# Kernel optimization log

Hardware: AMD Instinct MI355X
Metric: run time of the kernel (lower is better)

The kernel has to match this reference:

```python
import jax, jax.numpy as jnp
import numpy as np

DIM = 256
HID = 1024
BATCH = 16384
STEP_SIZE = 0.1
NSTEPS = 10  # int(1.0 / step_size)


def setup_inputs() -> dict:
    key = jax.random.key(0)
    ks = jax.random.split(key, 8)
    x = jax.random.normal(ks[0], (BATCH, DIM), dtype=jnp.float32)
    # Scaled init so tanh layers stay in a sane range (like default torch init).
    W1 = jax.random.normal(ks[1], (DIM + 1, HID), dtype=jnp.float32) / np.sqrt(DIM + 1)
    b1 = jnp.zeros((HID,), dtype=jnp.float32)
    W2 = jax.random.normal(ks[2], (HID, HID), dtype=jnp.float32) / np.sqrt(HID)
    b2 = jnp.zeros((HID,), dtype=jnp.float32)
    W3 = jax.random.normal(ks[3], (HID, DIM), dtype=jnp.float32) / np.sqrt(HID)
    b3 = jnp.zeros((DIM,), dtype=jnp.float32)
    proj_mat = jax.random.normal(ks[4], (DIM, DIM), dtype=jnp.float32)
    return {"x": x, "W1": W1, "b1": b1, "W2": W2, "b2": b2,
            "W3": W3, "b3": b3, "proj_mat": proj_mat}


def reference(x, W1, b1, W2, b2, W3, b3, proj_mat):
    """FlowProposal.log_prob: backward RK4 integration of dx/dt = v(x,t)
    from t=1 to t=0 with Hutchinson trace estimation via forward-mode JVP.
    Returns log q(x), shape [batch]."""
    dtype = x.dtype

    def net(xc, t):
        # VelocityMLP: concat(x, t) -> tanh MLP -> velocity [B, DIM]
        tcol = jnp.broadcast_to(jnp.asarray(t, dtype), (xc.shape[0], 1))
        h = jnp.tanh(jnp.concatenate([xc, tcol], axis=1) @ W1 + b1)
        h = jnp.tanh(h @ W2 + b2)
        return h @ W3 + b3

    # Deterministic hashed Hutchinson noise (from the INITIAL x, as in torch).
    noise = jnp.sin((x @ proj_mat) * 1000.0) * 1.41421356  # sqrt(2)

    def dyn(xc, t):
        v, jv = jax.jvp(lambda xi: net(xi, t), (xc,), (noise,))
        tr = jnp.sum(noise * jv, axis=1, keepdims=True)  # eps^T J eps, [B,1]
        return v, tr

    dt = -STEP_SIZE

    def step(carry, k):
        xt, ljt = carry
        t = 1.0 + dt * k
        v1, tr1 = dyn(xt, t)
        v2, tr2 = dyn(xt + dt * 0.5 * v1, t + dt * 0.5)
        v3, tr3 = dyn(xt + dt * 0.5 * v2, t + dt * 0.5)
        v4, tr4 = dyn(xt + dt * v3, t + dt)
        xt = xt + (dt / 6.0) * (v1 + 2 * v2 + 2 * v3 + v4)
        ljt = ljt + (dt / 6.0) * (tr1 + 2 * tr2 + 2 * tr3 + tr4)
        return (xt, ljt), None

    init = (x, jnp.zeros((x.shape[0], 1), dtype))
    (xt, ljt), _ = jax.lax.scan(step, init, jnp.arange(NSTEPS, dtype=dtype))

    log_prob_z = -0.5 * jnp.sum(xt * xt, axis=1) - 0.5 * DIM * jnp.log(jnp.asarray(2.0 * np.pi, dtype))
    return log_prob_z - ljt[:, 0]
```

## Files before the change

kernel.cpp:

```cpp
#include <hip/hip_runtime.h>
#include <stdint.h>
#include <stddef.h>

typedef unsigned short ushort_t;
typedef float f32x4 __attribute__((ext_vector_type(4)));
typedef short short8 __attribute__((ext_vector_type(8)));

#define NB 16384
#define DIMX 256
#define HIDX 1024
#define DTC (-0.1f)

__device__ __forceinline__ unsigned short f2bf_bits(float f){
  unsigned int u = __float_as_uint(f);
  unsigned int r = (u + 0x7FFFu + ((u >> 16) & 1u)) >> 16;
  return (unsigned short)r;
}
__device__ __forceinline__ float bf2f_bits(unsigned short s){
  return __uint_as_float(((unsigned int)s) << 16);
}
__device__ __forceinline__ float fast_tanh(float x){
  float a = fabsf(x);
  float e = __expf(a + a);
  float r = 1.0f - 2.0f / (e + 1.0f);
  return copysignf(r, x);
}
__device__ __forceinline__ void gload16(const void* g, void* l){
  __builtin_amdgcn_global_load_lds(
      (const __attribute__((address_space(1))) void*)g,
      (__attribute__((address_space(3))) void*)l, 16, 0, 0);
}
template<int N> __device__ __forceinline__ void wait_vmcnt(){
  if constexpr (N == 0)      asm volatile("s_waitcnt vmcnt(0)" ::: "memory");
  else if constexpr (N == 4) asm volatile("s_waitcnt vmcnt(4)" ::: "memory");
  else if constexpr (N == 6) asm volatile("s_waitcnt vmcnt(6)" ::: "memory");
  else if constexpr (N == 8) asm volatile("s_waitcnt vmcnt(8)" ::: "memory");
  else static_assert(N == 0, "unsupported vmcnt");
}
__device__ __forceinline__ int ldsx(int r, int c){
  return r * 64 + (c ^ ((r & 7) << 3));
}

__global__ void prep_weights(const float* __restrict__ W1, const float* __restrict__ W2,
                             const float* __restrict__ W3,
                             ushort_t* __restrict__ W1at, ushort_t* __restrict__ W2t,
                             ushort_t* __restrict__ W3t, ushort_t* __restrict__ W3n){
  int i = blockIdx.x * blockDim.x + threadIdx.x;
  const int T1 = 1024 * 256, T2 = 1024 * 1024, T3 = 256 * 1024, T4 = 1024 * 256;
  if (i < T1){
    int n = i >> 8, k = i & 255;
    W1at[i] = f2bf_bits(W1[k * 1024 + n]);
  } else if (i < T1 + T2){
    int j = i - T1; int n = j >> 10, k = j & 1023;
    W2t[j] = f2bf_bits(W2[k * 1024 + n]);
  } else if (i < T1 + T2 + T3){
    int j = i - T1 - T2; int n = j >> 10, k = j & 1023;
    W3t[j] = f2bf_bits(W3[k * 256 + n]);
  } else if (i < T1 + T2 + T3 + T4){
    int j = i - T1 - T2 - T3;
    W3n[j] = f2bf_bits(W3[j]);
  }
}

__global__ void noise_init(const float* __restrict__ x, const float* __restrict__ proj,
                           ushort_t* __restrict__ noise_bf,
                           float* __restrict__ xt, ushort_t* __restrict__ xcbf,
                           float* __restrict__ ljt){
  const int r0 = blockIdx.x * 8;
  const int j = threadIdx.x;
  __shared__ float xrow[8][256];
  #pragma unroll
  for (int r = 0; r < 8; ++r) xrow[r][j] = x[(size_t)(r0 + r) * 256 + j];
  __syncthreads();
  float s[8] = {0.f,0.f,0.f,0.f,0.f,0.f,0.f,0.f};
  for (int k = 0; k < 256; ++k){
    float p = proj[k * 256 + j];
    #pragma unroll
    for (int r = 0; r < 8; ++r) s[r] = fmaf(xrow[r][k], p, s[r]);
  }
  #pragma unroll
  for (int r = 0; r < 8; ++r){
    float nz = sinf(s[r] * 1000.0f) * 1.41421356237f;
    size_t idx = (size_t)(r0 + r) * 256 + j;
    noise_bf[idx] = f2bf_bits(nz);
    float xv = xrow[r][j];
    xt[idx] = xv;
    xcbf[idx] = f2bf_bits(xv);
  }
  if (j < 8) ljt[r0 + j] = 0.0f;
}

template<int BM, int BN, int WGM, int K, int DUAL, int EPI, int PIPE>
__launch_bounds__(512, 2)
__global__ void gemm_kernel(const ushort_t* __restrict__ A1, const ushort_t* __restrict__ A2,
                            const ushort_t* __restrict__ Wt,
                            ushort_t* __restrict__ out1, ushort_t* __restrict__ out2,
                            const float* __restrict__ bias, const float* __restrict__ w1trow,
                            float tval,
                            const ushort_t* __restrict__ dz1,
                            const ushort_t* __restrict__ gtr,
                            float* __restrict__ xt, float* __restrict__ vacc,
                            ushort_t* __restrict__ xcbf,
                            float* __restrict__ ljt, float wdt6, int rk){
  constexpr int BK = 64;
  constexpr int WGN = 8 / WGM;
  constexpr int WM = BM / WGM, WN = BN / WGN;
  constexpr int M_REP = WM / 16, N_REP = WN / 16;
  constexpr int ATILES = DUAL ? 2 : 1;
  constexpr int CH_A = BM / 8;
  constexpr int CH_TOT = ATILES * CH_A + BN / 8;
  constexpr int CH_PW = CH_TOT / 8;
  constexpr int BUF_E = (ATILES * BM + BN) * BK;
  constexpr int NBUF = PIPE ? 2 : 1;
  constexpr int NK = K / BK;
  static_assert(!PIPE || NK >= 2, "pipeline needs >=2 K-steps");

  __shared__ __align__(16) ushort_t lds[NBUF * BUF_E];

  const int m0 = blockIdx.x * BM;
  const int n0 = blockIdx.y * BN;
  const int tid = threadIdx.x;
  const int lane = tid & 63;
  const int wid = tid >> 6;
  const int wr = wid / WGN;
  const int wc = wid % WGN;

  f32x4 acc1[M_REP][N_REP] = {};
  f32x4 acc2[M_REP][N_REP] = {};

  const int srow = lane >> 3;
  const int scol = ((lane & 7) ^ srow) * 8;

  const ushort_t* srcb[CH_PW];
  #pragma unroll
  for (int c = 0; c < CH_PW; ++c){
    const int ch = wid * CH_PW + c;
    if (ch < CH_A)
      srcb[c] = A1 + (size_t)(m0 + ch * 8 + srow) * K + scol;
    else if (DUAL && ch < 2 * CH_A)
      srcb[c] = A2 + (size_t)(m0 + (ch - CH_A) * 8 + srow) * K + scol;
    else
      srcb[c] = Wt + (size_t)(n0 + (ch - ATILES * CH_A) * 8 + srow) * K + scol;
  }

  auto do_stage = [&](int buf, int ks){
    ushort_t* dst = lds + buf * BUF_E + (wid * CH_PW) * 512;
    const int k0 = ks * BK;
    #pragma unroll
    for (int c = 0; c < CH_PW; ++c)
      gload16(srcb[c] + k0, dst + c * 512);
  };

  auto compute = [&](int buf){
    const ushort_t* ldsA1 = lds + buf * BUF_E;
    const ushort_t* ldsA2 = ldsA1 + BM * BK;
    const ushort_t* ldsB  = ldsA1 + ATILES * BM * BK;
    #pragma unroll
    for (int kk = 0; kk < 2; ++kk){
      short8 a1f[M_REP], a2f[M_REP], bfr[N_REP];
      const int lco = kk * 32 + (lane >> 4) * 8;
      const int lro = lane & 15;
      #pragma unroll
      for (int m = 0; m < M_REP; ++m){
        int r = wr * WM + m * 16 + lro;
        a1f[m] = *(const short8*)(ldsA1 + ldsx(r, lco));
        if (DUAL) a2f[m] = *(const short8*)(ldsA2 + ldsx(r, lco));
      }
      #pragma unroll
      for (int n = 0; n < N_REP; ++n){
        int cN = wc * WN + n * 16 + lro;
        bfr[n] = *(const short8*)(ldsB + ldsx(cN, lco));
      }
      #pragma unroll
      for (int m = 0; m < M_REP; ++m){
        #pragma unroll
        for (int n = 0; n < N_REP; ++n){
          acc1[m][n] = __builtin_amdgcn_mfma_f32_16x16x32_bf16(a1f[m], bfr[n], acc1[m][n], 0, 0, 0);
          if (DUAL)
            acc2[m][n] = __builtin_amdgcn_mfma_f32_16x16x32_bf16(a2f[m], bfr[n], acc2[m][n], 0, 0, 0);
        }
      }
    }
  };

  if constexpr (PIPE){
    do_stage(0, 0);
    do_stage(1, 1);
    for (int ks = 0; ks < NK - 2; ++ks){
      wait_vmcnt<CH_PW>();
      __builtin_amdgcn_s_barrier();
      compute(ks & 1);
      asm volatile("s_waitcnt lgkmcnt(0)" ::: "memory");
      __builtin_amdgcn_s_barrier();
      do_stage(ks & 1, ks + 2);
    }
    wait_vmcnt<CH_PW>();
    __builtin_amdgcn_s_barrier();
    compute(NK & 1);
    wait_vmcnt<0>();
    __builtin_amdgcn_s_barrier();
    compute((NK - 1) & 1);
  } else {
    for (int ks = 0; ks < NK; ++ks){
      do_stage(0, ks);
      __syncthreads();
      compute(0);
      __syncthreads();
    }
  }

  const int rbase = (lane >> 4) * 4;
  const int cbase = lane & 15;
  if (EPI <= 1){
    #pragma unroll
    for (int m = 0; m < M_REP; ++m){
      #pragma unroll
      for (int n = 0; n < N_REP; ++n){
        #pragma unroll
        for (int j = 0; j < 4; ++j){
          const int R = m0 + wr * WM + m * 16 + rbase + j;
          const int C = n0 + wc * WN + n * 16 + cbase;
          const size_t idx = (size_t)R * HIDX + C;
          float a = acc1[m][n][j];
          if (EPI == 0){
            out1[idx] = f2bf_bits(a);
          } else {
            float z = a + bias[C] + tval * w1trow[C];
            float h = fast_tanh(z);
            out1[idx] = f2bf_bits(h);
            float d = bf2f_bits(dz1[idx]);
            out2[idx] = f2bf_bits(fmaf(-h, h, 1.0f) * d);
          }
        }
      }
    }
  } else if (EPI == 2){
    #pragma unroll
    for (int m = 0; m < M_REP; ++m){
      #pragma unroll
      for (int j = 0; j < 4; ++j){
        const int R = m0 + wr * WM + m * 16 + rbase + j;
        float psum = 0.0f;
        #pragma unroll
        for (int n = 0; n < N_REP; ++n){
          const int C = n0 + wc * WN + n * 16 + cbase;
          const size_t idx = (size_t)R * HIDX + C;
          float h = fast_tanh(acc1[m][n][j] + bias[C]);
          out1[idx] = f2bf_bits(h);
          float dh2 = fmaf(-h, h, 1.0f) * acc2[m][n][j];
          psum += dh2 * bf2f_bits(gtr[idx]);
        }
        #pragma unroll
        for (int off = 1; off < 16; off <<= 1) psum += __shfl_xor(psum, off, 64);
        if (cbase == 0) atomicAdd(&ljt[R], wdt6 * psum);
      }
    }
  } else {
    #pragma unroll
    for (int m = 0; m < M_REP; ++m){
      #pragma unroll
      for (int n = 0; n < N_REP; ++n){
        #pragma unroll
        for (int j = 0; j < 4; ++j){
          const int R = m0 + wr * WM + m * 16 + rbase + j;
          const int C = n0 + wc * WN + n * 16 + cbase;
          const size_t idx = (size_t)R * DIMX + C;
          float v = acc1[m][n][j] + bias[C];
          float xtv = xt[idx];
          if (rk == 0){
            vacc[idx] = v;
            xcbf[idx] = f2bf_bits(xtv + 0.5f * DTC * v);
          } else if (rk == 1){
            vacc[idx] += 2.0f * v;
            xcbf[idx] = f2bf_bits(xtv + 0.5f * DTC * v);
          } else if (rk == 2){
            vacc[idx] += 2.0f * v;
            xcbf[idx] = f2bf_bits(xtv + DTC * v);
          } else {
            float xtn = xtv + (DTC / 6.0f) * (vacc[idx] + v);
            xt[idx] = xtn;
            xcbf[idx] = f2bf_bits(xtn);
          }
        }
      }
    }
  }
}

__global__ void final_kernel(const float* __restrict__ xt, const float* __restrict__ ljt,
                             float* __restrict__ out){
  const int row = blockIdx.x * 4 + (threadIdx.x >> 6);
  const int lane = threadIdx.x & 63;
  const float4 xv = *(const float4*)(xt + (size_t)row * 256 + lane * 4);
  float s = xv.x * xv.x + xv.y * xv.y + xv.z * xv.z + xv.w * xv.w;
  #pragma unroll
  for (int off = 32; off; off >>= 1) s += __shfl_xor(s, off, 64);
  if (lane == 0) out[row] = -0.5f * s - 235.2482645f - ljt[row];
}

extern "C" void kernel_launch(void* const* d_in, const int* in_sizes, int n_in,
                              void* d_out, int out_size, void* d_ws, size_t ws_size,
                              hipStream_t stream){
  (void)in_sizes; (void)n_in; (void)out_size; (void)ws_size;
  const float* x    = (const float*)d_in[0];
  const float* W1   = (const float*)d_in[1];
  const float* b1   = (const float*)d_in[2];
  const float* W2   = (const float*)d_in[3];
  const float* b2   = (const float*)d_in[4];
  const float* W3   = (const float*)d_in[5];
  const float* b3   = (const float*)d_in[6];
  const float* proj = (const float*)d_in[7];

  size_t off = 0;
  char* wsb = (char*)d_ws;
  auto carve = [&](size_t n) -> char* {
    char* p = wsb + off; off += (n + 255) & ~(size_t)255; return p;
  };
  ushort_t* W1at     = (ushort_t*)carve((size_t)1024 * 256 * 2);
  ushort_t* W2t      = (ushort_t*)carve((size_t)1024 * 1024 * 2);
  ushort_t* W3t      = (ushort_t*)carve((size_t)256 * 1024 * 2);
  ushort_t* W3n      = (ushort_t*)carve((size_t)1024 * 256 * 2);
  ushort_t* noise_bf = (ushort_t*)carve((size_t)NB * 256 * 2);
  ushort_t* dz1      = (ushort_t*)carve((size_t)NB * 1024 * 2);
  ushort_t* gtr      = (ushort_t*)carve((size_t)NB * 1024 * 2);
  float*    xt       = (float*)carve((size_t)NB * 256 * 4);
  ushort_t* xcbf     = (ushort_t*)carve((size_t)NB * 256 * 2);
  float*    vacc     = (float*)carve((size_t)NB * 256 * 4);
  float*    ljt      = (float*)carve((size_t)NB * 4);
  ushort_t* h1       = (ushort_t*)carve((size_t)NB * 1024 * 2);
  ushort_t* dh1      = (ushort_t*)carve((size_t)NB * 1024 * 2);
  ushort_t* h2       = (ushort_t*)carve((size_t)NB * 1024 * 2);

  prep_weights<<<7168, 256, 0, stream>>>(W1, W2, W3, W1at, W2t, W3t, W3n);
  noise_init<<<NB / 8, 256, 0, stream>>>(x, proj, noise_bf, xt, xcbf, ljt);

  gemm_kernel<256, 256, 2, 256, 0, 0, 0><<<dim3(NB / 256, 4), 512, 0, stream>>>(
      noise_bf, nullptr, W1at, dz1, nullptr, nullptr, nullptr, 0.f,
      nullptr, nullptr, nullptr, nullptr, nullptr, nullptr, 0.f, 0);
  gemm_kernel<256, 256, 2, 256, 0, 0, 0><<<dim3(NB / 256, 4), 512, 0, stream>>>(
      noise_bf, nullptr, W3n, gtr, nullptr, nullptr, nullptr, 0.f,
      nullptr, nullptr, nullptr, nullptr, nullptr, nullptr, 0.f, 0);

  const float toff[4] = {0.0f, -0.05f, -0.05f, -0.1f};
  const float wst[4]  = {1.0f, 2.0f, 2.0f, 1.0f};
  for (int k = 0; k < 10; ++k){
    float t = 1.0f - 0.1f * (float)k;
    for (int s = 0; s < 4; ++s){
      gemm_kernel<256, 256, 2, 256, 0, 1, 0><<<dim3(NB / 256, 4), 512, 0, stream>>>(
          xcbf, nullptr, W1at, h1, dh1, b1, W1 + 256 * 1024, t + toff[s],
          dz1, nullptr, nullptr, nullptr, nullptr, nullptr, 0.f, 0);
      gemm_kernel<128, 256, 2, 1024, 1, 2, 1><<<dim3(NB / 128, 4), 512, 0, stream>>>(
          h1, dh1, W2t, h2, nullptr, b2, nullptr, 0.f,
          nullptr, gtr, nullptr, nullptr, nullptr, ljt, wst[s] * (DTC / 6.0f), 0);
      gemm_kernel<128, 128, 4, 1024, 0, 3, 0><<<dim3(NB / 128, 2), 512, 0, stream>>>(
          h2, nullptr, W3t, nullptr, nullptr, b3, nullptr, 0.f,
          nullptr, nullptr, xt, vacc, xcbf, nullptr, 0.f, s);
    }
  }
  final_kernel<<<NB / 4, 256, 0, stream>>>(xt, ljt, (float*)d_out);
}
```

Baseline: 5.661 ms.

## Add BK=32 pipelined path for dual-A W2 GEMM with smaller tiles, higher occupancy

Adds a new pipeline mode for the dual-input (h1, dh1) W2 GEMM that stages 32-wide K slices into a double-buffered LDS tile with a new XOR swizzle. The launch switches from 128x256 tiles to 128x128 tiles and doubles the grid, with launch bounds raised to allow four blocks per CU. The goal is to cut per-block LDS and registers so more blocks can be resident and hide latency. The cost is that each A tile is loaded twice as often across the N dimension, and there are more barriers per unit of K work.

```diff
diff --git a/kernel.cpp b/kernel.cpp
--- a/kernel.cpp
+++ b/kernel.cpp
@@ -32,6 +32,7 @@
 }
 template<int N> __device__ __forceinline__ void wait_vmcnt(){
   if constexpr (N == 0)      asm volatile("s_waitcnt vmcnt(0)" ::: "memory");
+  else if constexpr (N == 3) asm volatile("s_waitcnt vmcnt(3)" ::: "memory");
   else if constexpr (N == 4) asm volatile("s_waitcnt vmcnt(4)" ::: "memory");
   else if constexpr (N == 6) asm volatile("s_waitcnt vmcnt(6)" ::: "memory");
   else if constexpr (N == 8) asm volatile("s_waitcnt vmcnt(8)" ::: "memory");
@@ -39,6 +40,9 @@
 }
 __device__ __forceinline__ int ldsx(int r, int c){
   return r * 64 + (c ^ ((r & 7) << 3));
+}
+__device__ __forceinline__ int ldsx32(int r, int g){
+  return r * 32 + ((g ^ (r & 3) ^ ((r >> 2) & 3)) << 3);
 }
 
 __global__ void prep_weights(const float* __restrict__ W1, const float* __restrict__ W2,
@@ -91,7 +95,7 @@
 }
 
 template<int BM, int BN, int WGM, int K, int DUAL, int EPI, int PIPE>
-__launch_bounds__(512, 2)
+__launch_bounds__(512, (PIPE == 3) ? 4 : 2)
 __global__ void gemm_kernel(const ushort_t* __restrict__ A1, const ushort_t* __restrict__ A2,
                             const ushort_t* __restrict__ Wt,
                             ushort_t* __restrict__ out1, ushort_t* __restrict__ out2,
@@ -102,20 +106,11 @@
                             float* __restrict__ xt, float* __restrict__ vacc,
                             ushort_t* __restrict__ xcbf,
                             float* __restrict__ ljt, float wdt6, int rk){
-  constexpr int BK = 64;
   constexpr int WGN = 8 / WGM;
   constexpr int WM = BM / WGM, WN = BN / WGN;
   constexpr int M_REP = WM / 16, N_REP = WN / 16;
   constexpr int ATILES = DUAL ? 2 : 1;
-  constexpr int CH_A = BM / 8;
-  constexpr int CH_TOT = ATILES * CH_A + BN / 8;
-  constexpr int CH_PW = CH_TOT / 8;
-  constexpr int BUF_E = (ATILES * BM + BN) * BK;
-  constexpr int NBUF = PIPE ? 2 : 1;
-  constexpr int NK = K / BK;
-  static_assert(!PIPE || NK >= 2, "pipeline needs >=2 K-steps");
-
-  __shared__ __align__(16) ushort_t lds[NBUF * BUF_E];
+  constexpr int ROWS = ATILES * BM + BN;
 
   const int m0 = blockIdx.x * BM;
   const int n0 = blockIdx.y * BN;
@@ -128,84 +123,158 @@
   f32x4 acc1[M_REP][N_REP] = {};
   f32x4 acc2[M_REP][N_REP] = {};
 
-  const int srow = lane >> 3;
-  const int scol = ((lane & 7) ^ srow) * 8;
-
-  const ushort_t* srcb[CH_PW];
-  #pragma unroll
-  for (int c = 0; c < CH_PW; ++c){
-    const int ch = wid * CH_PW + c;
-    if (ch < CH_A)
-      srcb[c] = A1 + (size_t)(m0 + ch * 8 + srow) * K + scol;
-    else if (DUAL && ch < 2 * CH_A)
-      srcb[c] = A2 + (size_t)(m0 + (ch - CH_A) * 8 + srow) * K + scol;
-    else
-      srcb[c] = Wt + (size_t)(n0 + (ch - ATILES * CH_A) * 8 + srow) * K + scol;
-  }
-
-  auto do_stage = [&](int buf, int ks){
-    ushort_t* dst = lds + buf * BUF_E + (wid * CH_PW) * 512;
-    const int k0 = ks * BK;
-    #pragma unroll
-    for (int c = 0; c < CH_PW; ++c)
-      gload16(srcb[c] + k0, dst + c * 512);
-  };
-
-  auto compute = [&](int buf){
-    const ushort_t* ldsA1 = lds + buf * BUF_E;
-    const ushort_t* ldsA2 = ldsA1 + BM * BK;
-    const ushort_t* ldsB  = ldsA1 + ATILES * BM * BK;
-    #pragma unroll
-    for (int kk = 0; kk < 2; ++kk){
+  if constexpr (PIPE == 3){
+    constexpr int NT = K / 32;
+    constexpr int CH = ROWS / 16;
+    constexpr int CH_PW = CH / 8;
+    constexpr int BUF_E = ROWS * 32;
+    static_assert(CH_PW * 8 == CH, "chunk split");
+    __shared__ __align__(16) ushort_t lds[2 * BUF_E];
+
+    const int srow = lane >> 2;
+    const int scb  = (lane & 3) ^ (srow & 3) ^ ((srow >> 2) & 3);
+    const int scol = scb << 3;
+    const ushort_t* srcb[CH_PW];
+    #pragma unroll
+    for (int c = 0; c < CH_PW; ++c){
+      const int gr = (wid * CH_PW + c) * 16 + srow;
+      if (gr < BM)               srcb[c] = A1 + (size_t)(m0 + gr) * K + scol;
+      else if (DUAL && gr < 2 * BM) srcb[c] = A2 + (size_t)(m0 + gr - BM) * K + scol;
+      else                       srcb[c] = Wt + (size_t)(n0 + gr - ATILES * BM) * K + scol;
+    }
+    auto do_stage = [&](int buf, int t){
+      ushort_t* dst = lds + buf * BUF_E + (wid * CH_PW) * 512;
+      #pragma unroll
+      for (int c = 0; c < CH_PW; ++c)
+        gload16(srcb[c] + t * 32, dst + c * 512);
+    };
+    auto compute = [&](int buf){
+      const ushort_t* base = lds + buf * BUF_E;
+      const int g = lane >> 4;
+      const int lro = lane & 15;
       short8 a1f[M_REP], a2f[M_REP], bfr[N_REP];
-      const int lco = kk * 32 + (lane >> 4) * 8;
-      const int lro = lane & 15;
       #pragma unroll
       for (int m = 0; m < M_REP; ++m){
-        int r = wr * WM + m * 16 + lro;
-        a1f[m] = *(const short8*)(ldsA1 + ldsx(r, lco));
-        if (DUAL) a2f[m] = *(const short8*)(ldsA2 + ldsx(r, lco));
+        const int r = wr * WM + m * 16 + lro;
+        a1f[m] = *(const short8*)(base + ldsx32(r, g));
+        a2f[m] = *(const short8*)(base + ldsx32(BM + r, g));
       }
       #pragma unroll
       for (int n = 0; n < N_REP; ++n){
-        int cN = wc * WN + n * 16 + lro;
-        bfr[n] = *(const short8*)(ldsB + ldsx(cN, lco));
+        const int rn = ATILES * BM + wc * WN + n * 16 + lro;
+        bfr[n] = *(const short8*)(base + ldsx32(rn, g));
       }
       #pragma unroll
       for (int m = 0; m < M_REP; ++m){
         #pragma unroll
         for (int n = 0; n < N_REP; ++n){
           acc1[m][n] = __builtin_amdgcn_mfma_f32_16x16x32_bf16(a1f[m], bfr[n], acc1[m][n], 0, 0, 0);
-          if (DUAL)
-            acc2[m][n] = __builtin_amdgcn_mfma_f32_16x16x32_bf16(a2f[m], bfr[n], acc2[m][n], 0, 0, 0);
-        }
-      }
-    }
-  };
-
-  if constexpr (PIPE){
+          acc2[m][n] = __builtin_amdgcn_mfma_f32_16x16x32_bf16(a2f[m], bfr[n], acc2[m][n], 0, 0, 0);
+        }
+      }
+    };
     do_stage(0, 0);
     do_stage(1, 1);
-    for (int ks = 0; ks < NK - 2; ++ks){
+    for (int t = 0; t < NT - 2; ++t){
       wait_vmcnt<CH_PW>();
       __builtin_amdgcn_s_barrier();
-      compute(ks & 1);
+      compute(t & 1);
       asm volatile("s_waitcnt lgkmcnt(0)" ::: "memory");
       __builtin_amdgcn_s_barrier();
-      do_stage(ks & 1, ks + 2);
+      do_stage(t & 1, t + 2);
     }
     wait_vmcnt<CH_PW>();
     __builtin_amdgcn_s_barrier();
-    compute(NK & 1);
+    compute(NT & 1);
     wait_vmcnt<0>();
     __builtin_amdgcn_s_barrier();
-    compute((NK - 1) & 1);
+    compute((NT - 1) & 1);
   } else {
-    for (int ks = 0; ks < NK; ++ks){
-      do_stage(0, ks);
-      __syncthreads();
-      compute(0);
-      __syncthreads();
+    constexpr int BK = 64;
+    constexpr int CH_A = BM / 8;
+    constexpr int CH_TOT = ATILES * CH_A + BN / 8;
+    constexpr int CH_PW = CH_TOT / 8;
+    constexpr int BUF_E = ROWS * BK;
+    constexpr int NBUF = PIPE ? 2 : 1;
+    constexpr int NK = K / BK;
+    __shared__ __align__(16) ushort_t lds[NBUF * BUF_E];
+
+    const int srow = lane >> 3;
+    const int scol = ((lane & 7) ^ srow) * 8;
+    const ushort_t* srcb[CH_PW];
+    #pragma unroll
+    for (int c = 0; c < CH_PW; ++c){
+      const int ch = wid * CH_PW + c;
+      if (ch < CH_A)
+        srcb[c] = A1 + (size_t)(m0 + ch * 8 + srow) * K + scol;
+      else if (DUAL && ch < 2 * CH_A)
+        srcb[c] = A2 + (size_t)(m0 + (ch - CH_A) * 8 + srow) * K + scol;
+      else
+        srcb[c] = Wt + (size_t)(n0 + (ch - ATILES * CH_A) * 8 + srow) * K + scol;
+    }
+    auto do_stage = [&](int buf, int ks){
+      ushort_t* dst = lds + buf * BUF_E + (wid * CH_PW) * 512;
+      const int k0 = ks * BK;
+      #pragma unroll
+      for (int c = 0; c < CH_PW; ++c)
+        gload16(srcb[c] + k0, dst + c * 512);
+    };
+    auto compute = [&](int buf){
+      const ushort_t* ldsA1 = lds + buf * BUF_E;
+      const ushort_t* ldsA2 = ldsA1 + BM * BK;
+      const ushort_t* ldsB  = ldsA1 + ATILES * BM * BK;
+      #pragma unroll
+      for (int kk = 0; kk < 2; ++kk){
+        short8 a1f[M_REP], a2f[M_REP], bfr[N_REP];
+        const int lco = kk * 32 + (lane >> 4) * 8;
+        const int lro = lane & 15;
+        #pragma unroll
+        for (int m = 0; m < M_REP; ++m){
+          int r = wr * WM + m * 16 + lro;
+          a1f[m] = *(const short8*)(ldsA1 + ldsx(r, lco));
+          if (DUAL) a2f[m] = *(const short8*)(ldsA2 + ldsx(r, lco));
+        }
+        #pragma unroll
+        for (int n = 0; n < N_REP; ++n){
+          int cN = wc * WN + n * 16 + lro;
+          bfr[n] = *(const short8*)(ldsB + ldsx(cN, lco));
+        }
+        #pragma unroll
+        for (int m = 0; m < M_REP; ++m){
+          #pragma unroll
+          for (int n = 0; n < N_REP; ++n){
+            acc1[m][n] = __builtin_amdgcn_mfma_f32_16x16x32_bf16(a1f[m], bfr[n], acc1[m][n], 0, 0, 0);
+            if (DUAL)
+              acc2[m][n] = __builtin_amdgcn_mfma_f32_16x16x32_bf16(a2f[m], bfr[n], acc2[m][n], 0, 0, 0);
+          }
+        }
+      }
+    };
+
+    if constexpr (PIPE == 1){
+      do_stage(0, 0);
+      do_stage(1, 1);
+      for (int ks = 0; ks < NK - 2; ++ks){
+        wait_vmcnt<CH_PW>();
+        __builtin_amdgcn_s_barrier();
+        compute(ks & 1);
+        asm volatile("s_waitcnt lgkmcnt(0)" ::: "memory");
+        __builtin_amdgcn_s_barrier();
+        do_stage(ks & 1, ks + 2);
+      }
+      wait_vmcnt<CH_PW>();
+      __builtin_amdgcn_s_barrier();
+      compute(NK & 1);
+      wait_vmcnt<0>();
+      __builtin_amdgcn_s_barrier();
+      compute((NK - 1) & 1);
+    } else {
+      for (int ks = 0; ks < NK; ++ks){
+        do_stage(0, ks);
+        __syncthreads();
+        compute(0);
+        __syncthreads();
+      }
     }
   }
 
@@ -349,7 +418,7 @@
       gemm_kernel<256, 256, 2, 256, 0, 1, 0><<<dim3(NB / 256, 4), 512, 0, stream>>>(
           xcbf, nullptr, W1at, h1, dh1, b1, W1 + 256 * 1024, t + toff[s],
           dz1, nullptr, nullptr, nullptr, nullptr, nullptr, 0.f, 0);
-      gemm_kernel<128, 256, 2, 1024, 1, 2, 1><<<dim3(NB / 128, 4), 512, 0, stream>>>(
+      gemm_kernel<128, 128, 4, 1024, 1, 2, 3><<<dim3(NB / 128, 8), 512, 0, stream>>>(
           h1, dh1, W2t, h2, nullptr, b2, nullptr, 0.f,
           nullptr, gtr, nullptr, nullptr, nullptr, ljt, wst[s] * (DTC / 6.0f), 0);
       gemm_kernel<128, 128, 4, 1024, 0, 3, 0><<<dim3(NB / 128, 2), 512, 0, stream>>>(
```

Result: slower. 5.812 ms (+2.7%).
